# Kernel tuning notes

Measured on AMD Instinct MI355X. Metric: run time of the kernel, lower is better.

Reference implementation:

```python
import jax, jax.numpy as jnp
import numpy as np

N = 100000   # nodes
DEG = 32     # in-degree per node
E = N * DEG  # 3.2M edges
D = 24       # node feature dim
NK = 2       # number of anisotropic kernels (tile(...,2) in source forces 2)
H = 64       # MLP hidden/out channels


def setup_inputs() -> dict:
    key = jax.random.key(0)
    k1, k2, k3, k4 = jax.random.split(key, 4)
    x = jax.random.normal(k1, (N, D), dtype=jnp.float32)
    src = jax.random.randint(k2, (E,), 0, N)
    tgt = jnp.repeat(jnp.arange(N), DEG)  # every node has DEG in-edges -> no 0/0
    edge_index = jnp.stack([src, tgt]).astype(jnp.int64)
    kvals = jax.random.normal(k3, (NK, E), dtype=jnp.float32)
    # Linear(2*D -> H, bias=False), xavier-like scale
    W = jax.random.normal(k4, (H, NK * D), dtype=jnp.float32) * (1.0 / (NK * D))
    return {"x": x, "edge_index": edge_index, "kvals": kvals, "W": W}


def reference(x, edge_index, kvals, W):
    src, tgt = edge_index[0], edge_index[1]
    xs = x[src]  # [E, D] gathered source features
    # per-kernel sparse aggregation: out_k[i] = sum_{e: tgt[e]==i} kvals[k,e] * x[src[e]]
    out = jnp.concatenate(
        [jax.ops.segment_sum(kvals[k][:, None] * xs, tgt, num_segments=N)
         for k in range(NK)], axis=1)  # [N, NK*D]
    # adj_norm: subtract tiled neighbor mean
    deg = jax.ops.segment_sum(jnp.ones((E,), x.dtype), tgt, num_segments=N)  # [N]
    sum_x = jax.ops.segment_sum(xs, tgt, num_segments=N)  # [N, D]
    norm_x = sum_x / deg[:, None]
    out = out - jnp.tile(norm_x, (1, NK)) + jnp.tile(x, (1, NK))
    # MLP: single bias-free linear, no activation
    return out @ W.T  # [N, H]
```

## Files before the change

kernel.cpp:

```cpp
#include <hip/hip_runtime.h>


#define NN   100000
#define DEG  32
#define EE   (NN * DEG)
#define DD   24
#define HH   64
#define NPB  64
#define TPB  256
#define NPW  16

typedef __attribute__((ext_vector_type(8)))  short short8;
typedef __attribute__((ext_vector_type(16))) float float16;

__device__ __forceinline__ unsigned short f2bf(float f) {
    union { float f; unsigned u; } v; v.f = f;
    unsigned r = v.u + 0x7fffu + ((v.u >> 16) & 1u);
    return (unsigned short)(r >> 16);
}

__device__ __forceinline__ short8 pack8(unsigned g0, unsigned g1, unsigned g2, unsigned g3,
                                        unsigned g4, unsigned g5, unsigned g6, unsigned g7) {
    union { unsigned u[4]; short8 s; } p;
    p.u[0] = g0 | (g1 << 16);
    p.u[1] = g2 | (g3 << 16);
    p.u[2] = g4 | (g5 << 16);
    p.u[3] = g6 | (g7 << 16);
    return p.s;
}

__global__ void xcvt(const float* __restrict__ x, unsigned short* __restrict__ xb, int n4) {
    int i = blockIdx.x * blockDim.x + threadIdx.x;
    if (i < n4) {
        float4 v = ((const float4*)x)[i];
        ushort4 o;
        o.x = f2bf(v.x); o.y = f2bf(v.y); o.z = f2bf(v.z); o.w = f2bf(v.w);
        ((ushort4*)xb)[i] = o;
    }
}

__global__ __launch_bounds__(TPB, 4) void gnn(
    const float*          __restrict__ x,
    const unsigned short* __restrict__ xb,
    const int*            __restrict__ ei,
    const float*          __restrict__ kv,
    const float*          __restrict__ W,
    float*                __restrict__ out)
{
    __shared__ unsigned short pre_s[NPB * 48];

    const int t    = threadIdx.x;
    const int lane = t & 63;
    const int w    = t >> 6;
    const int m    = lane & 31;
    const int kh   = lane >> 5;
    const int base = blockIdx.x * NPB;
    const float* kv1 = kv + EE;
    const int dclamp = (m < DD) ? m : (DD - 1);

    #pragma unroll 2
    for (int i = 0; i < NPW; ++i) {
        const int nl = w * NPW + i;
        int node = base + nl; if (node >= NN) node = NN - 1;
        const int eb = node * DEG;

        float16 acc;
        #pragma unroll
        for (int r = 0; r < 16; ++r) acc[r] = 0.f;

        #pragma unroll
        for (int kc = 0; kc < 2; ++kc) {
            const int e0 = eb + kc * 16 + kh * 8;

            short8 afrag;
            if (m < 2) {
                const float* ar = (m == 0 ? kv : kv1) + e0;
                const float4 cA = ((const float4*)ar)[0];
                const float4 cB = ((const float4*)ar)[1];
                afrag = pack8(f2bf(cA.x), f2bf(cA.y), f2bf(cA.z), f2bf(cA.w),
                              f2bf(cB.x), f2bf(cB.y), f2bf(cB.z), f2bf(cB.w));
            } else if (m == 2) {
                unsigned one2 = 0x3F803F80u;
                union { unsigned u[4]; short8 s; } p;
                p.u[0] = one2; p.u[1] = one2; p.u[2] = one2; p.u[3] = one2;
                afrag = p.s;
            } else {
                union { unsigned u[4]; short8 s; } p;
                p.u[0] = 0; p.u[1] = 0; p.u[2] = 0; p.u[3] = 0;
                afrag = p.s;
            }

            const int4 sA = ((const int4*)(ei + e0))[0];
            const int4 sB = ((const int4*)(ei + e0))[1];
            const unsigned g0 = xb[sA.x * DD + dclamp];
            const unsigned g1 = xb[sA.y * DD + dclamp];
            const unsigned g2 = xb[sA.z * DD + dclamp];
            const unsigned g3 = xb[sA.w * DD + dclamp];
            const unsigned g4 = xb[sB.x * DD + dclamp];
            const unsigned g5 = xb[sB.y * DD + dclamp];
            const unsigned g6 = xb[sB.z * DD + dclamp];
            const unsigned g7 = xb[sB.w * DD + dclamp];
            const short8 bfrag = pack8(g0, g1, g2, g3, g4, g5, g6, g7);

            acc = __builtin_amdgcn_mfma_f32_32x32x16_bf16(afrag, bfrag, acc, 0, 0, 0);
        }

        if (kh == 0 && m < DD) {
            const float sm = acc[2] * (1.f / 32.f);
            const float xv = x[node * DD + m];
            pre_s[nl * 48 + m]      = f2bf(acc[0] - sm + xv);
            pre_s[nl * 48 + 24 + m] = f2bf(acc[1] - sm + xv);
        }
    }
    __syncthreads();

    {
        const int mt = w >> 1;
        const int nt = w & 1;
        const int h  = nt * 32 + m;

        float16 acc;
        #pragma unroll
        for (int r = 0; r < 16; ++r) acc[r] = 0.f;

        #pragma unroll
        for (int kc = 0; kc < 3; ++kc) {
            const int c0 = kc * 16 + kh * 8;
            const short8 af = *((const short8*)(pre_s + (mt * 32 + m) * 48 + c0));
            const float* wr = W + h * 48 + c0;
            const float4 wA = ((const float4*)wr)[0];
            const float4 wB = ((const float4*)wr)[1];
            const short8 bf = pack8(f2bf(wA.x), f2bf(wA.y), f2bf(wA.z), f2bf(wA.w),
                                    f2bf(wB.x), f2bf(wB.y), f2bf(wB.z), f2bf(wB.w));
            acc = __builtin_amdgcn_mfma_f32_32x32x16_bf16(af, bf, acc, 0, 0, 0);
        }

        #pragma unroll
        for (int r = 0; r < 16; ++r) {
            const int row = (r & 3) + 8 * (r >> 2) + 4 * kh;
            const int gn  = base + mt * 32 + row;
            if (gn < NN) out[gn * HH + h] = acc[r];
        }
    }
}

extern "C" void kernel_launch(void* const* d_in, const int* in_sizes, int n_in,
                              void* d_out, int out_size, void* d_ws, size_t ws_size,
                              hipStream_t stream) {
    const float* x  = (const float*)d_in[0];
    const int*   ei = (const int*)d_in[1];
    const float* kv = (const float*)d_in[2];
    const float* W  = (const float*)d_in[3];
    float* out = (float*)d_out;

    unsigned short* xb = (unsigned short*)d_ws;
    const int n4 = NN * DD / 4;
    xcvt<<<(n4 + 255) / 256, 256, 0, stream>>>(x, xb, n4);

    const int grid = (NN + NPB - 1) / NPB;
    gnn<<<grid, TPB, 0, stream>>>(x, xb, ei, kv, W, out);
}
```

Baseline: 153.1 us.

## Stage edge indices and kvals in LDS and software-pipeline neighbor gathers

Each block now loads its edge indices and both kernel-value rows with coalesced vector loads into shared memory, converting kvals to bf16 once, instead of reading them per MFMA lane. The per-node gather of neighbor features is double-buffered in registers so the next node's loads are issued before the current node's MFMAs. Blocks shrink to 32 nodes, which gives more blocks, and only two waves run the output projection. Bounds checks are dropped because 100000 divides evenly by 32. The intent is to hide gather latency and cut redundant global traffic, at the cost of higher register and LDS use, which may lower occupancy.

```diff
diff --git a/kernel.cpp b/kernel.cpp
--- a/kernel.cpp
+++ b/kernel.cpp
@@ -6,9 +6,9 @@
 #define EE   (NN * DEG)
 #define DD   24
 #define HH   64
-#define NPB  64
+#define NPB  32
 #define TPB  256
-#define NPW  16
+#define NPW  8
 
 typedef __attribute__((ext_vector_type(8)))  short short8;
 typedef __attribute__((ext_vector_type(16))) float float16;
@@ -26,6 +26,12 @@
     p.u[1] = g2 | (g3 << 16);
     p.u[2] = g4 | (g5 << 16);
     p.u[3] = g6 | (g7 << 16);
+    return p.s;
+}
+
+__device__ __forceinline__ short8 const8(unsigned v) {
+    union { unsigned u[4]; short8 s; } p;
+    p.u[0] = v; p.u[1] = v; p.u[2] = v; p.u[3] = v;
     return p.s;
 }
 
@@ -47,6 +53,8 @@
     const float*          __restrict__ W,
     float*                __restrict__ out)
 {
+    __shared__ int            ei_s[NPB * DEG];
+    __shared__ unsigned short kv_s[2 * NPB * DEG];
     __shared__ unsigned short pre_s[NPB * 48];
 
     const int t    = threadIdx.x;
@@ -54,70 +62,91 @@
     const int w    = t >> 6;
     const int m    = lane & 31;
     const int kh   = lane >> 5;
+    const int kh8  = kh * 8;
     const int base = blockIdx.x * NPB;
-    const float* kv1 = kv + EE;
     const int dclamp = (m < DD) ? m : (DD - 1);
 
-    #pragma unroll 2
+    {
+        const size_t eb = (size_t)base * DEG;
+        const int4 ev = ((const int4*)(ei + eb))[t];
+        ((int4*)ei_s)[t] = ev;
+        const float4 c0 = ((const float4*)(kv + eb))[t];
+        const float4 c1 = ((const float4*)(kv + EE + eb))[t];
+        ushort4 u0, u1;
+        u0.x = f2bf(c0.x); u0.y = f2bf(c0.y); u0.z = f2bf(c0.z); u0.w = f2bf(c0.w);
+        u1.x = f2bf(c1.x); u1.y = f2bf(c1.y); u1.z = f2bf(c1.z); u1.w = f2bf(c1.w);
+        ((ushort4*)kv_s)[t] = u0;
+        ((ushort4*)(kv_s + NPB * DEG))[t] = u1;
+    }
+    __syncthreads();
+
+    const unsigned short* kvrow = kv_s + (m & 1) * (NPB * DEG);
+
+    unsigned g[2][16];
+    float    xv[2];
+
+    #define LOAD_NODE(nl, sl) do {                                             \
+        const int el_ = (nl) * DEG + kh8;                                      \
+        const int4 s0_ = *(const int4*)(ei_s + el_);                           \
+        const int4 s1_ = *(const int4*)(ei_s + el_ + 4);                       \
+        const int4 s2_ = *(const int4*)(ei_s + el_ + 16);                      \
+        const int4 s3_ = *(const int4*)(ei_s + el_ + 20);                      \
+        g[sl][0]  = xb[s0_.x * DD + dclamp];                                   \
+        g[sl][1]  = xb[s0_.y * DD + dclamp];                                   \
+        g[sl][2]  = xb[s0_.z * DD + dclamp];                                   \
+        g[sl][3]  = xb[s0_.w * DD + dclamp];                                   \
+        g[sl][4]  = xb[s1_.x * DD + dclamp];                                   \
+        g[sl][5]  = xb[s1_.y * DD + dclamp];                                   \
+        g[sl][6]  = xb[s1_.z * DD + dclamp];                                   \
+        g[sl][7]  = xb[s1_.w * DD + dclamp];                                   \
+        g[sl][8]  = xb[s2_.x * DD + dclamp];                                   \
+        g[sl][9]  = xb[s2_.y * DD + dclamp];                                   \
+        g[sl][10] = xb[s2_.z * DD + dclamp];                                   \
+        g[sl][11] = xb[s2_.w * DD + dclamp];                                   \
+        g[sl][12] = xb[s3_.x * DD + dclamp];                                   \
+        g[sl][13] = xb[s3_.y * DD + dclamp];                                   \
+        g[sl][14] = xb[s3_.z * DD + dclamp];                                   \
+        g[sl][15] = xb[s3_.w * DD + dclamp];                                   \
+        xv[sl] = x[(base + (nl)) * DD + dclamp];                               \
+    } while (0)
+
+    LOAD_NODE(w * NPW, 0);
+
+    #pragma unroll
     for (int i = 0; i < NPW; ++i) {
-        const int nl = w * NPW + i;
-        int node = base + nl; if (node >= NN) node = NN - 1;
-        const int eb = node * DEG;
+        const int cur = i & 1;
+        const int nl  = w * NPW + i;
+        if (i < NPW - 1) LOAD_NODE(nl + 1, cur ^ 1);
+
+        const int el = nl * DEG + kh8;
+        short8 raw0 = *(const short8*)(kvrow + el);
+        short8 raw1 = *(const short8*)(kvrow + el + 16);
+        const short8 af0 = (m < 2) ? raw0 : const8(m == 2 ? 0x3F803F80u : 0u);
+        const short8 af1 = (m < 2) ? raw1 : const8(m == 2 ? 0x3F803F80u : 0u);
+
+        const short8 bf0 = pack8(g[cur][0], g[cur][1], g[cur][2],  g[cur][3],
+                                 g[cur][4], g[cur][5], g[cur][6],  g[cur][7]);
+        const short8 bf1 = pack8(g[cur][8], g[cur][9], g[cur][10], g[cur][11],
+                                 g[cur][12], g[cur][13], g[cur][14], g[cur][15]);
 
         float16 acc;
         #pragma unroll
         for (int r = 0; r < 16; ++r) acc[r] = 0.f;
-
-        #pragma unroll
-        for (int kc = 0; kc < 2; ++kc) {
-            const int e0 = eb + kc * 16 + kh * 8;
-
-            short8 afrag;
-            if (m < 2) {
-                const float* ar = (m == 0 ? kv : kv1) + e0;
-                const float4 cA = ((const float4*)ar)[0];
-                const float4 cB = ((const float4*)ar)[1];
-                afrag = pack8(f2bf(cA.x), f2bf(cA.y), f2bf(cA.z), f2bf(cA.w),
-                              f2bf(cB.x), f2bf(cB.y), f2bf(cB.z), f2bf(cB.w));
-            } else if (m == 2) {
-                unsigned one2 = 0x3F803F80u;
-                union { unsigned u[4]; short8 s; } p;
-                p.u[0] = one2; p.u[1] = one2; p.u[2] = one2; p.u[3] = one2;
-                afrag = p.s;
-            } else {
-                union { unsigned u[4]; short8 s; } p;
-                p.u[0] = 0; p.u[1] = 0; p.u[2] = 0; p.u[3] = 0;
-                afrag = p.s;
-            }
-
-            const int4 sA = ((const int4*)(ei + e0))[0];
-            const int4 sB = ((const int4*)(ei + e0))[1];
-            const unsigned g0 = xb[sA.x * DD + dclamp];
-            const unsigned g1 = xb[sA.y * DD + dclamp];
-            const unsigned g2 = xb[sA.z * DD + dclamp];
-            const unsigned g3 = xb[sA.w * DD + dclamp];
-            const unsigned g4 = xb[sB.x * DD + dclamp];
-            const unsigned g5 = xb[sB.y * DD + dclamp];
-            const unsigned g6 = xb[sB.z * DD + dclamp];
-            const unsigned g7 = xb[sB.w * DD + dclamp];
-            const short8 bfrag = pack8(g0, g1, g2, g3, g4, g5, g6, g7);
-
-            acc = __builtin_amdgcn_mfma_f32_32x32x16_bf16(afrag, bfrag, acc, 0, 0, 0);
-        }
+        acc = __builtin_amdgcn_mfma_f32_32x32x16_bf16(af0, bf0, acc, 0, 0, 0);
+        acc = __builtin_amdgcn_mfma_f32_32x32x16_bf16(af1, bf1, acc, 0, 0, 0);
 
         if (kh == 0 && m < DD) {
             const float sm = acc[2] * (1.f / 32.f);
-            const float xv = x[node * DD + m];
-            pre_s[nl * 48 + m]      = f2bf(acc[0] - sm + xv);
-            pre_s[nl * 48 + 24 + m] = f2bf(acc[1] - sm + xv);
+            const float pv = xv[cur] - sm;
+            pre_s[nl * 48 + m]      = f2bf(acc[0] + pv);
+            pre_s[nl * 48 + 24 + m] = f2bf(acc[1] + pv);
         }
     }
+    #undef LOAD_NODE
     __syncthreads();
 
-    {
-        const int mt = w >> 1;
-        const int nt = w & 1;
-        const int h  = nt * 32 + m;
+    if (w < 2) {
+        const int h = w * 32 + m;
 
         float16 acc;
         #pragma unroll
@@ -125,8 +154,8 @@
 
         #pragma unroll
         for (int kc = 0; kc < 3; ++kc) {
-            const int c0 = kc * 16 + kh * 8;
-            const short8 af = *((const short8*)(pre_s + (mt * 32 + m) * 48 + c0));
+            const int c0 = kc * 16 + kh8;
+            const short8 af = *(const short8*)(pre_s + m * 48 + c0);
             const float* wr = W + h * 48 + c0;
             const float4 wA = ((const float4*)wr)[0];
             const float4 wB = ((const float4*)wr)[1];
@@ -138,8 +167,7 @@
         #pragma unroll
         for (int r = 0; r < 16; ++r) {
             const int row = (r & 3) + 8 * (r >> 2) + 4 * kh;
-            const int gn  = base + mt * 32 + row;
-            if (gn < NN) out[gn * HH + h] = acc[r];
+            out[(size_t)(base + row) * HH + h] = acc[r];
         }
     }
 }
@@ -157,6 +185,6 @@
     const int n4 = NN * DD / 4;
     xcvt<<<(n4 + 255) / 256, 256, 0, stream>>>(x, xb, n4);
 
-    const int grid = (NN + NPB - 1) / NPB;
+    const int grid = NN / NPB;
     gnn<<<grid, TPB, 0, stream>>>(x, xb, ei, kv, W, out);
 }
```

Measured after the change: 127.9 us. 16.5% less time.
